# Optimization experiments

Measured on AMD Instinct MI355X. Metric: run time of the kernel, lower is better.

## Reference

```python
import jax, jax.numpy as jnp
import numpy as np

THETA = 0.5
STRIDE = 2
HEADS = 4
D_K = 32
D_V = 32
EPS = 1e-5


def pdc_conv(x, w, stride, theta=THETA):
    """Conv_PDC: (Co,Ci,1,8) weight -> 3x3 kernel with zero center, minus theta * 1x1 sum conv."""
    Co, Ci = w.shape[0], w.shape[1]
    w8 = w[:, :, 0, :]  # (Co, Ci, 8)
    w9 = jnp.concatenate(
        [w8[:, :, :4], jnp.zeros((Co, Ci, 1), w.dtype), w8[:, :, 4:]], axis=2
    ).reshape(Co, Ci, 3, 3)
    dn = jax.lax.conv_dimension_numbers(x.shape, w9.shape, ('NCHW', 'OIHW', 'NCHW'))
    out_n = jax.lax.conv_general_dilated(x, w9, (stride, stride), [(1, 1), (1, 1)], dimension_numbers=dn)
    kd = jnp.sum(w8, axis=2)[:, :, None, None]  # (Co, Ci, 1, 1)
    out_d = jax.lax.conv_general_dilated(x, kd, (stride, stride), [(0, 0), (0, 0)], dimension_numbers=dn)
    return out_n - theta * out_d


def full_layer_norm(x):
    # F.layer_norm(x, x.shape): normalize over ALL dims (incl. batch), no affine
    m = jnp.mean(x)
    v = jnp.mean(jnp.square(x - m))
    return (x - m) * jax.lax.rsqrt(v + EPS)


def setup_inputs() -> dict:
    key = jax.random.key(0)
    ks = jax.random.split(key, 12)
    b, c, h, w = 8, 64, 64, 64
    hd = HEADS * D_K  # 128
    s = 0.05
    return {
        'x': jax.random.normal(ks[0], (b, c, h, w), jnp.float32),
        'wk': jax.random.normal(ks[1], (c, c, 1, 8), jnp.float32) * s,
        'wv': jax.random.normal(ks[2], (c, c, 1, 8), jnp.float32) * s,
        'fcq_w': jax.random.normal(ks[3], (hd, c), jnp.float32) * s,
        'fcq_b': jax.random.normal(ks[4], (hd,), jnp.float32) * s,
        'fck_w': jax.random.normal(ks[5], (hd, c), jnp.float32) * s,
        'fck_b': jax.random.normal(ks[6], (hd,), jnp.float32) * s,
        'fcv_w': jax.random.normal(ks[7], (hd, c), jnp.float32) * s,
        'fcv_b': jax.random.normal(ks[8], (hd,), jnp.float32) * s,
        'fco_w': jax.random.normal(ks[9], (c, hd), jnp.float32) * s,
        'fco_b': jax.random.normal(ks[10], (c,), jnp.float32) * s,
        'B': jax.random.normal(ks[11], (1, HEADS, h * w, (h // STRIDE) * (w // STRIDE)), jnp.float32) * s,
    }


def reference(x, wk, wv, fcq_w, fcq_b, fck_w, fck_b, fcv_w, fcv_b, fco_w, fco_b, B):
    b, c, h, w = x.shape
    hw = h * w
    xr = jnp.transpose(x.reshape(b, c, hw), (0, 2, 1))  # (b, hw, c)
    xr = full_layer_norm(xr)

    q = xr @ fcq_w.T + fcq_b                    # (b, hw, H*dk)
    q = jnp.transpose(q.reshape(b, hw, HEADS, D_K), (0, 2, 1, 3))  # (b,H,hw,dk)

    k = pdc_conv(x, wk, STRIDE)                 # (b, c, h2, w2)
    kb, kc, kh, kw = k.shape
    k = jnp.transpose(k.reshape(kb, kc, kh * kw), (0, 2, 1)) @ fck_w.T + fck_b
    k = jnp.transpose(k.reshape(kb, kh * kw, HEADS, D_K), (0, 2, 1, 3))  # (b,H,n2,dk)

    v = pdc_conv(x, wv, STRIDE)
    vb, vc, vh, vw = v.shape
    v = jnp.transpose(v.reshape(vb, vc, vh * vw), (0, 2, 1)) @ fcv_w.T + fcv_b
    v = jnp.transpose(v.reshape(vb, vh * vw, HEADS, D_V), (0, 2, 1, 3))  # (b,H,n2,dv)

    attn = jnp.einsum('bhid,bhjd->bhij', q, k) * (D_K ** -0.5) + B
    attn = jax.nn.softmax(attn, axis=-1)
    out = jnp.einsum('bhij,bhjd->bhid', attn, v)            # (b,H,hw,dv)
    out = jnp.transpose(out, (0, 2, 1, 3)).reshape(b, hw, HEADS * D_V)
    out = out @ fco_w.T + fco_b                              # (b, hw, c)
    # Faithful to source: .view(b, channels, h, w) without permute
    out = out.reshape(b, c, h, w)
    return out + x
```

## Files before the change

### kernel.cpp

```cpp
#include <hip/hip_runtime.h>
#include <cmath>

#define THETA 0.5f
#define EPS 1e-5f

typedef __attribute__((ext_vector_type(8))) short bf16x8;
typedef __attribute__((ext_vector_type(4))) float f32x4;
typedef __attribute__((ext_vector_type(4))) unsigned u32x4;

__device__ inline unsigned short f2b(float f) {
  unsigned u = __builtin_bit_cast(unsigned, f);
  return (unsigned short)((u + 0x7fffu + ((u >> 16) & 1u)) >> 16);
}
__device__ inline float b2f(unsigned short u) {
  unsigned v = (unsigned)u << 16;
  return __builtin_bit_cast(float, v);
}
__device__ inline float blo(unsigned u) { return __builtin_bit_cast(float, u << 16); }
__device__ inline float bhi(unsigned u) { return __builtin_bit_cast(float, u & 0xffff0000u); }
__device__ inline float exp2fast(float x) {
  float r;
  asm("v_exp_f32 %0, %1" : "=v"(r) : "v"(x));
  return r;
}
__device__ inline unsigned cvtpk(float lo, float hi) {
  unsigned r;
  asm("v_cvt_pk_bf16_f32 %0, %1, %2" : "=v"(r) : "v"(lo), "v"(hi));
  return r;
}

__global__ __launch_bounds__(256) void pre_kernel(
    const float* __restrict__ B, unsigned short* __restrict__ B2, int nB4,
    const float* __restrict__ x, float* __restrict__ stats, int nx4) {
  int bx = blockIdx.x;
  if (bx < 2048) {
    int tid = bx * 256 + threadIdx.x;
    int stride = 2048 * 256;
    const float4* b4 = (const float4*)B;
    const float L = 1.4426950408889634f;
    for (int i = tid; i < nB4; i += stride) {
      float4 v = b4[i];
      unsigned lo = f2b(v.x * L) | ((unsigned)f2b(v.y * L) << 16);
      unsigned hi = f2b(v.z * L) | ((unsigned)f2b(v.w * L) << 16);
      *(uint2*)(B2 + (size_t)i * 4) = make_uint2(lo, hi);
    }
  } else {
    int sb = bx - 2048;
    int tid = sb * 256 + threadIdx.x;
    int stride = 512 * 256;
    float s = 0.f, ss = 0.f;
    const float4* x4 = (const float4*)x;
    for (int i = tid; i < nx4; i += stride) {
      float4 v = x4[i];
      s  += v.x + v.y + v.z + v.w;
      ss += v.x * v.x + v.y * v.y + v.z * v.z + v.w * v.w;
    }
    for (int off = 32; off; off >>= 1) {
      s  += __shfl_down(s, off);
      ss += __shfl_down(ss, off);
    }
    __shared__ float ls[4], lss[4];
    int lane = threadIdx.x & 63, wid = threadIdx.x >> 6;
    if (lane == 0) { ls[wid] = s; lss[wid] = ss; }
    __syncthreads();
    if (threadIdx.x == 0) {
      float a = 0.f, b = 0.f;
      for (int w = 0; w < 4; ++w) { a += ls[w]; b += lss[w]; }
      stats[2 * sb]     = a;
      stats[2 * sb + 1] = b;
    }
  }
}

__global__ __launch_bounds__(256) void pdc_conv_kernel(
    const float* __restrict__ x,
    const float* __restrict__ wk,
    const float* __restrict__ wv,
    float* __restrict__ Kc,
    float* __restrict__ Vc) {
  int oh  = blockIdx.x;
  int coh = blockIdx.y;
  int bb  = blockIdx.z;
  __shared__ float xs[64][3][64];
  const float* xb = x + (size_t)bb * 262144;
  int r1 = 2 * oh;
  for (int i = 0; i < 48; ++i) {
    int idx = threadIdx.x + i * 256;
    int ci = idx / 192;
    int rem = idx - ci * 192;
    int r = rem >> 6, col = rem & 63;
    int row = r1 - 1 + r;
    xs[ci][r][col] = (row >= 0) ? xb[((size_t)ci * 64 + row) * 64 + col] : 0.f;
  }
  __syncthreads();
  int owl = threadIdx.x & 7;
  int co  = coh * 32 + (threadIdx.x >> 3);
  int c0 = owl * 8;
  int ecol = c0 ? c0 - 1 : 0;
  float accK[4] = {0.f, 0.f, 0.f, 0.f}, accV[4] = {0.f, 0.f, 0.f, 0.f};
  const float* wkc = wk + (size_t)co * 512;
  const float* wvc = wv + (size_t)co * 512;
  for (int ci = 0; ci < 64; ++ci) {
    float4 k0 = *(const float4*)(wkc + ci * 8);
    float4 k1 = *(const float4*)(wkc + ci * 8 + 4);
    float4 v0 = *(const float4*)(wvc + ci * 8);
    float4 v1 = *(const float4*)(wvc + ci * 8 + 4);
    float kdk = k0.x + k0.y + k0.z + k0.w + k1.x + k1.y + k1.z + k1.w;
    float kdv = v0.x + v0.y + v0.z + v0.w + v1.x + v1.y + v1.z + v1.w;
    float wK[9] = {k0.x, k0.y, k0.z, k0.w, -THETA * kdk, k1.x, k1.y, k1.z, k1.w};
    float wV[9] = {v0.x, v0.y, v0.z, v0.w, -THETA * kdv, v1.x, v1.y, v1.z, v1.w};
    float xr[3][9];
#pragma unroll
    for (int r = 0; r < 3; ++r) {
      float ev = owl ? xs[ci][r][ecol] : 0.f;
      float4 a = *(const float4*)&xs[ci][r][c0];
      float4 b = *(const float4*)&xs[ci][r][c0 + 4];
      xr[r][0] = ev;
      xr[r][1] = a.x; xr[r][2] = a.y; xr[r][3] = a.z; xr[r][4] = a.w;
      xr[r][5] = b.x; xr[r][6] = b.y; xr[r][7] = b.z; xr[r][8] = b.w;
    }
#pragma unroll
    for (int ky = 0; ky < 3; ++ky)
#pragma unroll
      for (int kx = 0; kx < 3; ++kx) {
        float wkk = wK[ky * 3 + kx], wvv = wV[ky * 3 + kx];
#pragma unroll
        for (int i = 0; i < 4; ++i) {
          float xv = xr[ky][2 * i + kx];
          accK[i] = fmaf(wkk, xv, accK[i]);
          accV[i] = fmaf(wvv, xv, accV[i]);
        }
      }
  }
  size_t o = ((size_t)bb * 64 + co) * 1024 + oh * 32 + owl * 4;
  *(float4*)&Kc[o] = make_float4(accK[0], accK[1], accK[2], accK[3]);
  *(float4*)&Vc[o] = make_float4(accV[0], accV[1], accV[2], accV[3]);
}

__global__ __launch_bounds__(256) void proj_mfma_kernel(
    const float* __restrict__ x, const float* __restrict__ Kc, const float* __restrict__ Vc,
    const float* __restrict__ Wq, const float* __restrict__ bq,
    const float* __restrict__ Wk, const float* __restrict__ bk,
    const float* __restrict__ Wv, const float* __restrict__ bv,
    unsigned short* __restrict__ Qb, unsigned short* __restrict__ Kb,
    unsigned short* __restrict__ Vtb, const float* __restrict__ stats) {
  int bx = blockIdx.x;
  const float* A; const float* W; const float* bias; unsigned short* outp;
  int R, doLN, transp, r0, bb;
  if (bx < 512) {
    A = x; W = Wq; bias = bq; outp = Qb; R = 4096; doLN = 1; transp = 0;
    bb = bx >> 6; r0 = (bx & 63) * 64;
  } else {
    int i = bx - 512; int kv = i >> 7; int j = i & 127;
    bb = j >> 4; r0 = (j & 15) * 64; R = 1024; doLN = 0;
    if (!kv) { A = Kc; W = Wk; bias = bk; outp = Kb;  transp = 0; }
    else     { A = Vc; W = Wv; bias = bv; outp = Vtb; transp = 1; }
  }
  int tid = threadIdx.x;
  int w = tid >> 6, lane = tid & 63, g = lane >> 4, li = lane & 15;

  float m = 0.f, rs = 1.f;
  if (doLN) {
    const float2* sp = (const float2*)stats;
    float2 a = sp[tid];
    float2 b2 = sp[tid + 256];
    float s = a.x + b2.x, ss = a.y + b2.y;
    for (int off = 32; off; off >>= 1) {
      s  += __shfl_down(s, off);
      ss += __shfl_down(ss, off);
    }
    __shared__ float red[8];
    int lane0 = tid & 63, wid0 = tid >> 6;
    if (lane0 == 0) { red[wid0] = s; red[4 + wid0] = ss; }
    __syncthreads();
    float ts  = red[0] + red[1] + red[2] + red[3];
    float tss = red[4] + red[5] + red[6] + red[7];
    const float inv = 1.0f / 2097152.0f;
    m = ts * inv;
    float v = tss * inv - m * m;
    rs = rsqrtf(v + EPS);
    __syncthreads();
  }

  bf16x8 wf[2][2];
#pragma unroll
  for (int dd = 0; dd < 2; ++dd)
#pragma unroll
    for (int kh = 0; kh < 2; ++kh) {
      const float* wp = W + (size_t)(w * 32 + dd * 16 + li) * 64 + kh * 32 + g * 8;
      float4 w0 = *(const float4*)wp;
      float4 w1 = *(const float4*)(wp + 4);
      u32x4 u;
      u[0] = cvtpk(w0.x, w0.y); u[1] = cvtpk(w0.z, w0.w);
      u[2] = cvtpk(w1.x, w1.y); u[3] = cvtpk(w1.z, w1.w);
      wf[dd][kh] = __builtin_bit_cast(bf16x8, u);
    }

  __shared__ __align__(16) unsigned short As2[64][72];
  const float* Ab = A + (size_t)bb * 64 * R;
  for (int i = 0; i < 16; ++i) {
    int idx = tid + i * 256;
    int c = idx >> 6, r = idx & 63;
    float v = Ab[(size_t)c * R + r0 + r];
    if (doLN) v = (v - m) * rs;
    As2[r][c] = f2b(v);
  }
  __syncthreads();

  f32x4 acc[2][4];
#pragma unroll
  for (int dd = 0; dd < 2; ++dd)
#pragma unroll
    for (int rt = 0; rt < 4; ++rt) acc[dd][rt] = (f32x4){0.f, 0.f, 0.f, 0.f};

#pragma unroll
  for (int rt = 0; rt < 4; ++rt) {
    bf16x8 xf0 = *(const bf16x8*)&As2[rt * 16 + li][g * 8];
    bf16x8 xf1 = *(const bf16x8*)&As2[rt * 16 + li][32 + g * 8];
    if (!transp) {
#pragma unroll
      for (int dd = 0; dd < 2; ++dd) {
        acc[dd][rt] = __builtin_amdgcn_mfma_f32_16x16x32_bf16(wf[dd][0], xf0, acc[dd][rt], 0, 0, 0);
        acc[dd][rt] = __builtin_amdgcn_mfma_f32_16x16x32_bf16(wf[dd][1], xf1, acc[dd][rt], 0, 0, 0);
      }
    } else {
#pragma unroll
      for (int dd = 0; dd < 2; ++dd) {
        acc[dd][rt] = __builtin_amdgcn_mfma_f32_16x16x32_bf16(xf0, wf[dd][0], acc[dd][rt], 0, 0, 0);
        acc[dd][rt] = __builtin_amdgcn_mfma_f32_16x16x32_bf16(xf1, wf[dd][1], acc[dd][rt], 0, 0, 0);
      }
    }
  }

  size_t bh = (size_t)bb * 4 + w;
  if (!transp) {
#pragma unroll
    for (int dd = 0; dd < 2; ++dd) {
      float4 b4 = *(const float4*)(bias + w * 32 + dd * 16 + g * 4);
#pragma unroll
      for (int rt = 0; rt < 4; ++rt) {
        f32x4 a = acc[dd][rt];
        unsigned lo = cvtpk(a[0] + b4.x, a[1] + b4.y);
        unsigned hi = cvtpk(a[2] + b4.z, a[3] + b4.w);
        int r = r0 + rt * 16 + li;
        *(uint2*)(outp + (bh * R + r) * 32 + dd * 16 + g * 4) = make_uint2(lo, hi);
      }
    }
  } else {
#pragma unroll
    for (int dd = 0; dd < 2; ++dd) {
      float bsc = bias[w * 32 + dd * 16 + li];
#pragma unroll
      for (int rt = 0; rt < 4; ++rt) {
        f32x4 a = acc[dd][rt];
        unsigned lo = cvtpk(a[0] + bsc, a[1] + bsc);
        unsigned hi = cvtpk(a[2] + bsc, a[3] + bsc);
        *(uint2*)(outp + (bh * 32 + dd * 16 + li) * (size_t)R + r0 + rt * 16 + g * 4) =
            make_uint2(lo, hi);
      }
    }
  }
}

__global__ __launch_bounds__(256, 4) void attn_mfma_kernel(
    const unsigned short* __restrict__ Qb,
    const unsigned short* __restrict__ Kb,
    const unsigned short* __restrict__ Vtb,
    const unsigned short* __restrict__ B2,
    unsigned short* __restrict__ Ob) {
  int qt = blockIdx.x;
  int b  = blockIdx.y & 7;
  int h  = blockIdx.y >> 3;
  int tid = threadIdx.x;
  int w = tid >> 6, lane = tid & 63, g = lane >> 4, li = lane & 15;

  __shared__ __align__(16) unsigned short Ks[4096];
  __shared__ __align__(16) unsigned short Vs[4096];

  size_t bh = (size_t)b * 4 + h;
  int q0 = qt * 128 + w * 32;
  bf16x8 qfA = *(const bf16x8*)(Qb + (bh * 4096 + q0 + li) * 32 + g * 8);
  bf16x8 qfB = *(const bf16x8*)(Qb + (bh * 4096 + q0 + 16 + li) * 32 + g * 8);
  const unsigned short* BpA = B2 + ((size_t)h * 4096 + q0 + li) * 1024;
  const unsigned short* BpB = BpA + 16 * 1024;
  const unsigned short* Kg = Kb + bh * 32768;
  const unsigned short* Vg = Vtb + bh * 32768;

  float rsumA = 0.f, rsumB = 0.f;
  f32x4 accA0 = {0.f, 0.f, 0.f, 0.f}, accA1 = {0.f, 0.f, 0.f, 0.f};
  f32x4 accB0 = {0.f, 0.f, 0.f, 0.f}, accB1 = {0.f, 0.f, 0.f, 0.f};
  const float scale2 = 0.17677669529663687f * 1.4426950408889634f;

  int krow = tid >> 1, khalf = tid & 1;
  int j5 = krow & 31;
  int jp = (krow & ~31) | (((j5 >> 2) & 1) << 4) | (((j5 >> 3) & 3) << 2) | (j5 & 3);
  const int kc0 = ((jp >> 4) * 64 + khalf * 32 + (jp & 15)) * 8;
  int vr = tid >> 3, sg = tid & 7;
  const int vc0 = (((sg >> 1) * 2 + (vr >> 4)) * 64 + (sg & 1) * 32 + (vr & 15)) * 8;

  for (int jc = 0; jc < 1024; jc += 128) {
    __syncthreads();
    {
      const uint4* ks = (const uint4*)(Kg + (size_t)(jc + krow) * 32 + khalf * 16);
      *(uint4*)&Ks[kc0]       = ks[0];
      *(uint4*)&Ks[kc0 + 128] = ks[1];
      const uint4* vs = (const uint4*)(Vg + (size_t)vr * 1024 + jc + sg * 16);
      *(uint4*)&Vs[vc0]       = vs[0];
      *(uint4*)&Vs[vc0 + 128] = vs[1];
    }
    __syncthreads();

#pragma unroll
    for (int js = 0; js < 4; ++js) {
      bf16x8 kf0 = *(const bf16x8*)&Ks[((js * 2) * 64 + lane) * 8];
      bf16x8 kf1 = *(const bf16x8*)&Ks[((js * 2 + 1) * 64 + lane) * 8];
      const f32x4 z = {0.f, 0.f, 0.f, 0.f};
      f32x4 sA0 = __builtin_amdgcn_mfma_f32_16x16x32_bf16(kf0, qfA, z, 0, 0, 0);
      f32x4 sB0 = __builtin_amdgcn_mfma_f32_16x16x32_bf16(kf0, qfB, z, 0, 0, 0);
      f32x4 sA1 = __builtin_amdgcn_mfma_f32_16x16x32_bf16(kf1, qfA, z, 0, 0, 0);
      f32x4 sB1 = __builtin_amdgcn_mfma_f32_16x16x32_bf16(kf1, qfB, z, 0, 0, 0);

      u32x4 bA = *(const u32x4*)(BpA + jc + js * 32 + g * 8);
      u32x4 bB = *(const u32x4*)(BpB + jc + js * 32 + g * 8);

      float pA[8], pB[8];
      pA[0] = exp2fast(fmaf(sA0[0], scale2, blo(bA[0])));
      pA[1] = exp2fast(fmaf(sA0[1], scale2, bhi(bA[0])));
      pA[2] = exp2fast(fmaf(sA0[2], scale2, blo(bA[1])));
      pA[3] = exp2fast(fmaf(sA0[3], scale2, bhi(bA[1])));
      pA[4] = exp2fast(fmaf(sA1[0], scale2, blo(bA[2])));
      pA[5] = exp2fast(fmaf(sA1[1], scale2, bhi(bA[2])));
      pA[6] = exp2fast(fmaf(sA1[2], scale2, blo(bA[3])));
      pA[7] = exp2fast(fmaf(sA1[3], scale2, bhi(bA[3])));
      pB[0] = exp2fast(fmaf(sB0[0], scale2, blo(bB[0])));
      pB[1] = exp2fast(fmaf(sB0[1], scale2, bhi(bB[0])));
      pB[2] = exp2fast(fmaf(sB0[2], scale2, blo(bB[1])));
      pB[3] = exp2fast(fmaf(sB0[3], scale2, bhi(bB[1])));
      pB[4] = exp2fast(fmaf(sB1[0], scale2, blo(bB[2])));
      pB[5] = exp2fast(fmaf(sB1[1], scale2, bhi(bB[2])));
      pB[6] = exp2fast(fmaf(sB1[2], scale2, blo(bB[3])));
      pB[7] = exp2fast(fmaf(sB1[3], scale2, bhi(bB[3])));

      rsumA += ((pA[0] + pA[1]) + (pA[2] + pA[3])) + ((pA[4] + pA[5]) + (pA[6] + pA[7]));
      rsumB += ((pB[0] + pB[1]) + (pB[2] + pB[3])) + ((pB[4] + pB[5]) + (pB[6] + pB[7]));

      u32x4 wA, wB;
      wA[0] = cvtpk(pA[0], pA[1]); wA[1] = cvtpk(pA[2], pA[3]);
      wA[2] = cvtpk(pA[4], pA[5]); wA[3] = cvtpk(pA[6], pA[7]);
      wB[0] = cvtpk(pB[0], pB[1]); wB[1] = cvtpk(pB[2], pB[3]);
      wB[2] = cvtpk(pB[4], pB[5]); wB[3] = cvtpk(pB[6], pB[7]);
      bf16x8 paA = __builtin_bit_cast(bf16x8, wA);
      bf16x8 paB = __builtin_bit_cast(bf16x8, wB);

      bf16x8 vf0 = *(const bf16x8*)&Vs[(js * 128 + lane) * 8];
      bf16x8 vf1 = *(const bf16x8*)&Vs[((js * 2 + 1) * 64 + lane) * 8];
      accA0 = __builtin_amdgcn_mfma_f32_16x16x32_bf16(paA, vf0, accA0, 0, 0, 0);
      accA1 = __builtin_amdgcn_mfma_f32_16x16x32_bf16(paA, vf1, accA1, 0, 0, 0);
      accB0 = __builtin_amdgcn_mfma_f32_16x16x32_bf16(paB, vf0, accB0, 0, 0, 0);
      accB1 = __builtin_amdgcn_mfma_f32_16x16x32_bf16(paB, vf1, accB1, 0, 0, 0);
    }
  }

  rsumA += __shfl_xor(rsumA, 16);
  rsumA += __shfl_xor(rsumA, 32);
  rsumB += __shfl_xor(rsumB, 16);
  rsumB += __shfl_xor(rsumB, 32);
  float invA = 1.0f / rsumA;
  float invB = 1.0f / rsumB;
  float invqA[4], invqB[4];
#pragma unroll
  for (int r = 0; r < 4; ++r) {
    invqA[r] = __shfl(invA, g * 4 + r);
    invqB[r] = __shfl(invB, g * 4 + r);
  }

#pragma unroll
  for (int r = 0; r < 4; ++r) {
    size_t rowA = (size_t)b * 4096 + q0 + g * 4 + r;
    Ob[rowA * 128 + h * 32 + li]      = f2b(accA0[r] * invqA[r]);
    Ob[rowA * 128 + h * 32 + 16 + li] = f2b(accA1[r] * invqA[r]);
    size_t rowB = rowA + 16;
    Ob[rowB * 128 + h * 32 + li]      = f2b(accB0[r] * invqB[r]);
    Ob[rowB * 128 + h * 32 + 16 + li] = f2b(accB1[r] * invqB[r]);
  }
}

__global__ __launch_bounds__(256) void outproj_mfma_kernel(
    const unsigned short* __restrict__ O,
    const float* __restrict__ Wo,
    const float* __restrict__ bo,
    const float* __restrict__ x,
    float* __restrict__ out) {
  int pb = blockIdx.x & 127;
  int bb = blockIdx.x >> 7;
  int tid = threadIdx.x;
  int w = tid >> 6, lane = tid & 63, g = lane >> 4, li = lane & 15;
  int p0 = pb * 32;

  bf16x8 wf[4];
#pragma unroll
  for (int kt = 0; kt < 4; ++kt) {
    const float* wp = Wo + (size_t)(w * 16 + li) * 128 + kt * 32 + g * 8;
    float4 w0 = *(const float4*)wp;
    float4 w1 = *(const float4*)(wp + 4);
    u32x4 u;
    u[0] = cvtpk(w0.x, w0.y); u[1] = cvtpk(w0.z, w0.w);
    u[2] = cvtpk(w1.x, w1.y); u[3] = cvtpk(w1.z, w1.w);
    wf[kt] = __builtin_bit_cast(bf16x8, u);
  }

  f32x4 acc[2];
#pragma unroll
  for (int pt = 0; pt < 2; ++pt) acc[pt] = (f32x4){0.f, 0.f, 0.f, 0.f};

#pragma unroll
  for (int pt = 0; pt < 2; ++pt) {
    const unsigned short* Op = O + ((size_t)bb * 4096 + p0 + pt * 16 + li) * 128;
    bf16x8 of0 = *(const bf16x8*)(Op + g * 8);
    bf16x8 of1 = *(const bf16x8*)(Op + 32 + g * 8);
    bf16x8 of2 = *(const bf16x8*)(Op + 64 + g * 8);
    bf16x8 of3 = *(const bf16x8*)(Op + 96 + g * 8);
    acc[pt] = __builtin_amdgcn_mfma_f32_16x16x32_bf16(wf[0], of0, acc[pt], 0, 0, 0);
    acc[pt] = __builtin_amdgcn_mfma_f32_16x16x32_bf16(wf[1], of1, acc[pt], 0, 0, 0);
    acc[pt] = __builtin_amdgcn_mfma_f32_16x16x32_bf16(wf[2], of2, acc[pt], 0, 0, 0);
    acc[pt] = __builtin_amdgcn_mfma_f32_16x16x32_bf16(wf[3], of3, acc[pt], 0, 0, 0);
  }

  float4 bo4 = *(const float4*)(bo + w * 16 + g * 4);
#pragma unroll
  for (int pt = 0; pt < 2; ++pt) {
    int p = p0 + pt * 16 + li;
    size_t base = (size_t)bb * 262144 + (size_t)p * 64 + w * 16 + g * 4;
    float4 xr = *(const float4*)(x + base);
    float4 o;
    o.x = acc[pt][0] + bo4.x + xr.x;
    o.y = acc[pt][1] + bo4.y + xr.y;
    o.z = acc[pt][2] + bo4.z + xr.z;
    o.w = acc[pt][3] + bo4.w + xr.w;
    *(float4*)(out + base) = o;
  }
}

extern "C" void kernel_launch(void* const* d_in, const int* in_sizes, int n_in,
                              void* d_out, int out_size, void* d_ws, size_t ws_size,
                              hipStream_t stream) {
  const float* x    = (const float*)d_in[0];
  const float* wk   = (const float*)d_in[1];
  const float* wv   = (const float*)d_in[2];
  const float* fcqw = (const float*)d_in[3];
  const float* fcqb = (const float*)d_in[4];
  const float* fckw = (const float*)d_in[5];
  const float* fckb = (const float*)d_in[6];
  const float* fcvw = (const float*)d_in[7];
  const float* fcvb = (const float*)d_in[8];
  const float* fcow = (const float*)d_in[9];
  const float* fcob = (const float*)d_in[10];
  const float* Bb   = (const float*)d_in[11];
  float* out = (float*)d_out;
  float* ws  = (float*)d_ws;

  float* stats = ws;
  float* Kc = ws + 1024;
  float* Vc = Kc + 524288;
  unsigned short* B2  = (unsigned short*)(Vc + 524288);
  unsigned short* Qb  = B2 + 16777216;
  unsigned short* Kb  = Qb + 4194304;
  unsigned short* Vtb = Kb + 1048576;
  unsigned short* Ob  = Vtb + 1048576;

  pre_kernel<<<dim3(2560), dim3(256), 0, stream>>>(Bb, B2, 4194304, x, stats, 524288);
  pdc_conv_kernel<<<dim3(32, 2, 8), dim3(256), 0, stream>>>(x, wk, wv, Kc, Vc);
  proj_mfma_kernel<<<dim3(768), dim3(256), 0, stream>>>(
      x, Kc, Vc, fcqw, fcqb, fckw, fckb, fcvw, fcvb, Qb, Kb, Vtb, stats);
  attn_mfma_kernel<<<dim3(32, 32), dim3(256), 0, stream>>>(Qb, Kb, Vtb, B2, Ob);
  outproj_mfma_kernel<<<dim3(1024), dim3(256), 0, stream>>>(Ob, fcow, fcob, x, out);
}
```

Before: 229.0 us.

## Fuse PDC conv with K/V projection using bf16 MFMA implicit GEMM

Replaces the scalar fp32 PDC convolution kernel with an MFMA implicit-GEMM conv that reads bf16-transposed input tiles from LDS. The conv is fused with the K/V linear projections, so the fp32 Kc/Vc intermediates no longer round-trip through global memory. Conv weights are pre-packed to bf16 in extra blocks of the pre kernel, and the Q projection becomes its own specialised kernel. The cost is bf16 rounding of the conv inputs and weights, plus an intermediate bf16 rounding of the conv output before projection, which may reduce accuracy.

```diff
diff --git a/kernel.cpp b/kernel.cpp
--- a/kernel.cpp
+++ b/kernel.cpp
@@ -31,7 +31,9 @@
 
 __global__ __launch_bounds__(256) void pre_kernel(
     const float* __restrict__ B, unsigned short* __restrict__ B2, int nB4,
-    const float* __restrict__ x, float* __restrict__ stats, int nx4) {
+    const float* __restrict__ x, float* __restrict__ stats, int nx4,
+    const float* __restrict__ wk, const float* __restrict__ wv,
+    unsigned short* __restrict__ w9t) {
   int bx = blockIdx.x;
   if (bx < 2048) {
     int tid = bx * 256 + threadIdx.x;
@@ -44,7 +46,7 @@
       unsigned hi = f2b(v.z * L) | ((unsigned)f2b(v.w * L) << 16);
       *(uint2*)(B2 + (size_t)i * 4) = make_uint2(lo, hi);
     }
-  } else {
+  } else if (bx < 2560) {
     int sb = bx - 2048;
     int tid = sb * 256 + threadIdx.x;
     int stride = 512 * 256;
@@ -69,125 +71,159 @@
       stats[2 * sb]     = a;
       stats[2 * sb + 1] = b;
     }
-  }
-}
-
-__global__ __launch_bounds__(256) void pdc_conv_kernel(
+  } else {
+    int t = (bx - 2560) * 256 + threadIdx.x;
+    int kern = t >> 12, co = (t >> 6) & 63, ci = t & 63;
+    const float* w8 = (kern ? wv : wk) + ((size_t)co * 64 + ci) * 8;
+    float4 a = *(const float4*)w8;
+    float4 b = *(const float4*)(w8 + 4);
+    float s = (a.x + a.y + a.z + a.w) + (b.x + b.y + b.z + b.w);
+    unsigned short* o = w9t + (size_t)(kern * 64 + co) * 576 + ci;
+    o[0]       = f2b(a.x);
+    o[64]      = f2b(a.y);
+    o[128]     = f2b(a.z);
+    o[192]     = f2b(a.w);
+    o[256]     = f2b(-THETA * s);
+    o[320]     = f2b(b.x);
+    o[384]     = f2b(b.y);
+    o[448]     = f2b(b.z);
+    o[512]     = f2b(b.w);
+  }
+}
+
+__global__ __launch_bounds__(256) void convproj_kernel(
     const float* __restrict__ x,
-    const float* __restrict__ wk,
-    const float* __restrict__ wv,
-    float* __restrict__ Kc,
-    float* __restrict__ Vc) {
-  int oh  = blockIdx.x;
-  int coh = blockIdx.y;
-  int bb  = blockIdx.z;
-  __shared__ float xs[64][3][64];
-  const float* xb = x + (size_t)bb * 262144;
-  int r1 = 2 * oh;
-  for (int i = 0; i < 48; ++i) {
-    int idx = threadIdx.x + i * 256;
-    int ci = idx / 192;
-    int rem = idx - ci * 192;
-    int r = rem >> 6, col = rem & 63;
-    int row = r1 - 1 + r;
-    xs[ci][r][col] = (row >= 0) ? xb[((size_t)ci * 64 + row) * 64 + col] : 0.f;
-  }
-  __syncthreads();
-  int owl = threadIdx.x & 7;
-  int co  = coh * 32 + (threadIdx.x >> 3);
-  int c0 = owl * 8;
-  int ecol = c0 ? c0 - 1 : 0;
-  float accK[4] = {0.f, 0.f, 0.f, 0.f}, accV[4] = {0.f, 0.f, 0.f, 0.f};
-  const float* wkc = wk + (size_t)co * 512;
-  const float* wvc = wv + (size_t)co * 512;
-  for (int ci = 0; ci < 64; ++ci) {
-    float4 k0 = *(const float4*)(wkc + ci * 8);
-    float4 k1 = *(const float4*)(wkc + ci * 8 + 4);
-    float4 v0 = *(const float4*)(wvc + ci * 8);
-    float4 v1 = *(const float4*)(wvc + ci * 8 + 4);
-    float kdk = k0.x + k0.y + k0.z + k0.w + k1.x + k1.y + k1.z + k1.w;
-    float kdv = v0.x + v0.y + v0.z + v0.w + v1.x + v1.y + v1.z + v1.w;
-    float wK[9] = {k0.x, k0.y, k0.z, k0.w, -THETA * kdk, k1.x, k1.y, k1.z, k1.w};
-    float wV[9] = {v0.x, v0.y, v0.z, v0.w, -THETA * kdv, v1.x, v1.y, v1.z, v1.w};
-    float xr[3][9];
-#pragma unroll
-    for (int r = 0; r < 3; ++r) {
-      float ev = owl ? xs[ci][r][ecol] : 0.f;
-      float4 a = *(const float4*)&xs[ci][r][c0];
-      float4 b = *(const float4*)&xs[ci][r][c0 + 4];
-      xr[r][0] = ev;
-      xr[r][1] = a.x; xr[r][2] = a.y; xr[r][3] = a.z; xr[r][4] = a.w;
-      xr[r][5] = b.x; xr[r][6] = b.y; xr[r][7] = b.z; xr[r][8] = b.w;
-    }
-#pragma unroll
-    for (int ky = 0; ky < 3; ++ky)
-#pragma unroll
-      for (int kx = 0; kx < 3; ++kx) {
-        float wkk = wK[ky * 3 + kx], wvv = wV[ky * 3 + kx];
-#pragma unroll
-        for (int i = 0; i < 4; ++i) {
-          float xv = xr[ky][2 * i + kx];
-          accK[i] = fmaf(wkk, xv, accK[i]);
-          accV[i] = fmaf(wvv, xv, accV[i]);
-        }
-      }
-  }
-  size_t o = ((size_t)bb * 64 + co) * 1024 + oh * 32 + owl * 4;
-  *(float4*)&Kc[o] = make_float4(accK[0], accK[1], accK[2], accK[3]);
-  *(float4*)&Vc[o] = make_float4(accV[0], accV[1], accV[2], accV[3]);
-}
-
-__global__ __launch_bounds__(256) void proj_mfma_kernel(
-    const float* __restrict__ x, const float* __restrict__ Kc, const float* __restrict__ Vc,
-    const float* __restrict__ Wq, const float* __restrict__ bq,
+    const unsigned short* __restrict__ w9t,
     const float* __restrict__ Wk, const float* __restrict__ bk,
     const float* __restrict__ Wv, const float* __restrict__ bv,
-    unsigned short* __restrict__ Qb, unsigned short* __restrict__ Kb,
-    unsigned short* __restrict__ Vtb, const float* __restrict__ stats) {
-  int bx = blockIdx.x;
-  const float* A; const float* W; const float* bias; unsigned short* outp;
-  int R, doLN, transp, r0, bb;
-  if (bx < 512) {
-    A = x; W = Wq; bias = bq; outp = Qb; R = 4096; doLN = 1; transp = 0;
-    bb = bx >> 6; r0 = (bx & 63) * 64;
-  } else {
-    int i = bx - 512; int kv = i >> 7; int j = i & 127;
-    bb = j >> 4; r0 = (j & 15) * 64; R = 1024; doLN = 0;
-    if (!kv) { A = Kc; W = Wk; bias = bk; outp = Kb;  transp = 0; }
-    else     { A = Vc; W = Wv; bias = bv; outp = Vtb; transp = 1; }
-  }
+    unsigned short* __restrict__ Kb,
+    unsigned short* __restrict__ Vtb) {
+  int owh = blockIdx.x & 1;
+  int oh  = (blockIdx.x >> 1) & 31;
+  int bb  = blockIdx.x >> 6;
   int tid = threadIdx.x;
   int w = tid >> 6, lane = tid & 63, g = lane >> 4, li = lane & 15;
 
-  float m = 0.f, rs = 1.f;
-  if (doLN) {
-    const float2* sp = (const float2*)stats;
-    float2 a = sp[tid];
-    float2 b2 = sp[tid + 256];
-    float s = a.x + b2.x, ss = a.y + b2.y;
-    for (int off = 32; off; off >>= 1) {
-      s  += __shfl_down(s, off);
-      ss += __shfl_down(ss, off);
-    }
-    __shared__ float red[8];
-    int lane0 = tid & 63, wid0 = tid >> 6;
-    if (lane0 == 0) { red[wid0] = s; red[4 + wid0] = ss; }
-    __syncthreads();
-    float ts  = red[0] + red[1] + red[2] + red[3];
-    float tss = red[4] + red[5] + red[6] + red[7];
-    const float inv = 1.0f / 2097152.0f;
-    m = ts * inv;
-    float v = tss * inv - m * m;
-    rs = rsqrtf(v + EPS);
-    __syncthreads();
-  }
+  __shared__ __align__(16) unsigned short xsT[3][36][72];
+  __shared__ __align__(16) unsigned short ctK[16][72];
+  __shared__ __align__(16) unsigned short ctV[16][72];
+
+  const float* xb = x + (size_t)bb * 262144;
+  int g0 = owh * 32 - 4;
+  int rbase = 2 * oh - 1;
+  for (int i = 0; i < 27; ++i) {
+    int idx = tid + i * 256;
+    int ci = idx / 108;
+    int rem = idx - ci * 108;
+    int rr = rem / 36, cc = rem - rr * 36;
+    int row = rbase + rr, col = g0 + cc;
+    float v = (row >= 0 && col >= 0) ? xb[((size_t)ci * 64 + row) * 64 + col] : 0.f;
+    xsT[rr][cc][ci] = f2b(v);
+  }
+  __syncthreads();
+
+  f32x4 aK = {0.f, 0.f, 0.f, 0.f}, aV = {0.f, 0.f, 0.f, 0.f};
+#pragma unroll
+  for (int t = 0; t < 9; ++t) {
+    int ky = t / 3, kx = t - ky * 3;
+    int cc = 2 * li + 3 + kx;
+#pragma unroll
+    for (int kh = 0; kh < 2; ++kh) {
+      bf16x8 bfrag = *(const bf16x8*)&xsT[ky][cc][kh * 32 + g * 8];
+      bf16x8 ak = *(const bf16x8*)(w9t + (size_t)(w * 16 + li) * 576 + t * 64 + kh * 32 + g * 8);
+      bf16x8 av = *(const bf16x8*)(w9t + (size_t)(64 + w * 16 + li) * 576 + t * 64 + kh * 32 + g * 8);
+      aK = __builtin_amdgcn_mfma_f32_16x16x32_bf16(ak, bfrag, aK, 0, 0, 0);
+      aV = __builtin_amdgcn_mfma_f32_16x16x32_bf16(av, bfrag, aV, 0, 0, 0);
+    }
+  }
+  *(uint2*)&ctK[li][w * 16 + g * 4] = make_uint2(cvtpk(aK[0], aK[1]), cvtpk(aK[2], aK[3]));
+  *(uint2*)&ctV[li][w * 16 + g * 4] = make_uint2(cvtpk(aV[0], aV[1]), cvtpk(aV[2], aV[3]));
+  __syncthreads();
+
+  bf16x8 wfK[2][2], wfV[2][2];
+#pragma unroll
+  for (int dd = 0; dd < 2; ++dd)
+#pragma unroll
+    for (int kh = 0; kh < 2; ++kh) {
+      const float* wp = Wk + (size_t)(w * 32 + dd * 16 + li) * 64 + kh * 32 + g * 8;
+      float4 w0 = *(const float4*)wp;
+      float4 w1 = *(const float4*)(wp + 4);
+      u32x4 u;
+      u[0] = cvtpk(w0.x, w0.y); u[1] = cvtpk(w0.z, w0.w);
+      u[2] = cvtpk(w1.x, w1.y); u[3] = cvtpk(w1.z, w1.w);
+      wfK[dd][kh] = __builtin_bit_cast(bf16x8, u);
+      const float* vp = Wv + (size_t)(w * 32 + dd * 16 + li) * 64 + kh * 32 + g * 8;
+      float4 v0 = *(const float4*)vp;
+      float4 v1 = *(const float4*)(vp + 4);
+      u[0] = cvtpk(v0.x, v0.y); u[1] = cvtpk(v0.z, v0.w);
+      u[2] = cvtpk(v1.x, v1.y); u[3] = cvtpk(v1.z, v1.w);
+      wfV[dd][kh] = __builtin_bit_cast(bf16x8, u);
+    }
+
+  f32x4 pK[2] = {{0.f, 0.f, 0.f, 0.f}, {0.f, 0.f, 0.f, 0.f}};
+  f32x4 pV[2] = {{0.f, 0.f, 0.f, 0.f}, {0.f, 0.f, 0.f, 0.f}};
+#pragma unroll
+  for (int kh = 0; kh < 2; ++kh) {
+    bf16x8 bK  = *(const bf16x8*)&ctK[li][kh * 32 + g * 8];
+    bf16x8 aVc = *(const bf16x8*)&ctV[li][kh * 32 + g * 8];
+#pragma unroll
+    for (int dd = 0; dd < 2; ++dd) {
+      pK[dd] = __builtin_amdgcn_mfma_f32_16x16x32_bf16(wfK[dd][kh], bK, pK[dd], 0, 0, 0);
+      pV[dd] = __builtin_amdgcn_mfma_f32_16x16x32_bf16(aVc, wfV[dd][kh], pV[dd], 0, 0, 0);
+    }
+  }
+
+  size_t bh = (size_t)bb * 4 + w;
+  int pos0 = oh * 32 + owh * 16;
+#pragma unroll
+  for (int dd = 0; dd < 2; ++dd) {
+    float4 b4 = *(const float4*)(bk + w * 32 + dd * 16 + g * 4);
+    uint2 st = make_uint2(cvtpk(pK[dd][0] + b4.x, pK[dd][1] + b4.y),
+                          cvtpk(pK[dd][2] + b4.z, pK[dd][3] + b4.w));
+    *(uint2*)(Kb + (bh * 1024 + pos0 + li) * 32 + dd * 16 + g * 4) = st;
+    float bsc = bv[w * 32 + dd * 16 + li];
+    uint2 sv = make_uint2(cvtpk(pV[dd][0] + bsc, pV[dd][1] + bsc),
+                          cvtpk(pV[dd][2] + bsc, pV[dd][3] + bsc));
+    *(uint2*)(Vtb + (bh * 32 + dd * 16 + li) * 1024 + pos0 + g * 4) = sv;
+  }
+}
+
+__global__ __launch_bounds__(256) void projq_kernel(
+    const float* __restrict__ x, const float* __restrict__ Wq,
+    const float* __restrict__ bq, unsigned short* __restrict__ Qb,
+    const float* __restrict__ stats) {
+  int bx = blockIdx.x;
+  int bb = bx >> 6, r0 = (bx & 63) * 64;
+  const int R = 4096;
+  int tid = threadIdx.x;
+  int w = tid >> 6, lane = tid & 63, g = lane >> 4, li = lane & 15;
+
+  const float2* sp = (const float2*)stats;
+  float2 a = sp[tid];
+  float2 b2 = sp[tid + 256];
+  float s = a.x + b2.x, ss = a.y + b2.y;
+  for (int off = 32; off; off >>= 1) {
+    s  += __shfl_down(s, off);
+    ss += __shfl_down(ss, off);
+  }
+  __shared__ float red[8];
+  int lane0 = tid & 63, wid0 = tid >> 6;
+  if (lane0 == 0) { red[wid0] = s; red[4 + wid0] = ss; }
+  __syncthreads();
+  float ts  = red[0] + red[1] + red[2] + red[3];
+  float tss = red[4] + red[5] + red[6] + red[7];
+  const float inv = 1.0f / 2097152.0f;
+  float m = ts * inv;
+  float v0 = tss * inv - m * m;
+  float rs = rsqrtf(v0 + EPS);
+  __syncthreads();
 
   bf16x8 wf[2][2];
 #pragma unroll
   for (int dd = 0; dd < 2; ++dd)
 #pragma unroll
     for (int kh = 0; kh < 2; ++kh) {
-      const float* wp = W + (size_t)(w * 32 + dd * 16 + li) * 64 + kh * 32 + g * 8;
+      const float* wp = Wq + (size_t)(w * 32 + dd * 16 + li) * 64 + kh * 32 + g * 8;
       float4 w0 = *(const float4*)wp;
       float4 w1 = *(const float4*)(wp + 4);
       u32x4 u;
@@ -197,13 +233,12 @@
     }
 
   __shared__ __align__(16) unsigned short As2[64][72];
-  const float* Ab = A + (size_t)bb * 64 * R;
+  const float* Ab = x + (size_t)bb * 64 * R;
   for (int i = 0; i < 16; ++i) {
     int idx = tid + i * 256;
     int c = idx >> 6, r = idx & 63;
     float v = Ab[(size_t)c * R + r0 + r];
-    if (doLN) v = (v - m) * rs;
-    As2[r][c] = f2b(v);
+    As2[r][c] = f2b((v - m) * rs);
   }
   __syncthreads();
 
@@ -217,47 +252,24 @@
   for (int rt = 0; rt < 4; ++rt) {
     bf16x8 xf0 = *(const bf16x8*)&As2[rt * 16 + li][g * 8];
     bf16x8 xf1 = *(const bf16x8*)&As2[rt * 16 + li][32 + g * 8];
-    if (!transp) {
-#pragma unroll
-      for (int dd = 0; dd < 2; ++dd) {
-        acc[dd][rt] = __builtin_amdgcn_mfma_f32_16x16x32_bf16(wf[dd][0], xf0, acc[dd][rt], 0, 0, 0);
-        acc[dd][rt] = __builtin_amdgcn_mfma_f32_16x16x32_bf16(wf[dd][1], xf1, acc[dd][rt], 0, 0, 0);
-      }
-    } else {
-#pragma unroll
-      for (int dd = 0; dd < 2; ++dd) {
-        acc[dd][rt] = __builtin_amdgcn_mfma_f32_16x16x32_bf16(xf0, wf[dd][0], acc[dd][rt], 0, 0, 0);
-        acc[dd][rt] = __builtin_amdgcn_mfma_f32_16x16x32_bf16(xf1, wf[dd][1], acc[dd][rt], 0, 0, 0);
-      }
+#pragma unroll
+    for (int dd = 0; dd < 2; ++dd) {
+      acc[dd][rt] = __builtin_amdgcn_mfma_f32_16x16x32_bf16(wf[dd][0], xf0, acc[dd][rt], 0, 0, 0);
+      acc[dd][rt] = __builtin_amdgcn_mfma_f32_16x16x32_bf16(wf[dd][1], xf1, acc[dd][rt], 0, 0, 0);
     }
   }
 
   size_t bh = (size_t)bb * 4 + w;
-  if (!transp) {
-#pragma unroll
-    for (int dd = 0; dd < 2; ++dd) {
-      float4 b4 = *(const float4*)(bias + w * 32 + dd * 16 + g * 4);
-#pragma unroll
-      for (int rt = 0; rt < 4; ++rt) {
-        f32x4 a = acc[dd][rt];
-        unsigned lo = cvtpk(a[0] + b4.x, a[1] + b4.y);
-        unsigned hi = cvtpk(a[2] + b4.z, a[3] + b4.w);
-        int r = r0 + rt * 16 + li;
-        *(uint2*)(outp + (bh * R + r) * 32 + dd * 16 + g * 4) = make_uint2(lo, hi);
-      }
-    }
-  } else {
-#pragma unroll
-    for (int dd = 0; dd < 2; ++dd) {
-      float bsc = bias[w * 32 + dd * 16 + li];
-#pragma unroll
-      for (int rt = 0; rt < 4; ++rt) {
-        f32x4 a = acc[dd][rt];
-        unsigned lo = cvtpk(a[0] + bsc, a[1] + bsc);
-        unsigned hi = cvtpk(a[2] + bsc, a[3] + bsc);
-        *(uint2*)(outp + (bh * 32 + dd * 16 + li) * (size_t)R + r0 + rt * 16 + g * 4) =
-            make_uint2(lo, hi);
-      }
+#pragma unroll
+  for (int dd = 0; dd < 2; ++dd) {
+    float4 b4 = *(const float4*)(bq + w * 32 + dd * 16 + g * 4);
+#pragma unroll
+    for (int rt = 0; rt < 4; ++rt) {
+      f32x4 a2 = acc[dd][rt];
+      unsigned lo = cvtpk(a2[0] + b4.x, a2[1] + b4.y);
+      unsigned hi = cvtpk(a2[2] + b4.z, a2[3] + b4.w);
+      int r = r0 + rt * 16 + li;
+      *(uint2*)(Qb + (bh * (size_t)R + r) * 32 + dd * 16 + g * 4) = make_uint2(lo, hi);
     }
   }
 }
@@ -460,18 +472,18 @@
   float* ws  = (float*)d_ws;
 
   float* stats = ws;
-  float* Kc = ws + 1024;
-  float* Vc = Kc + 524288;
-  unsigned short* B2  = (unsigned short*)(Vc + 524288);
+  unsigned short* w9t = (unsigned short*)(ws + 1024);
+  unsigned short* B2  = w9t + 73728;
   unsigned short* Qb  = B2 + 16777216;
   unsigned short* Kb  = Qb + 4194304;
   unsigned short* Vtb = Kb + 1048576;
   unsigned short* Ob  = Vtb + 1048576;
 
-  pre_kernel<<<dim3(2560), dim3(256), 0, stream>>>(Bb, B2, 4194304, x, stats, 524288);
-  pdc_conv_kernel<<<dim3(32, 2, 8), dim3(256), 0, stream>>>(x, wk, wv, Kc, Vc);
-  proj_mfma_kernel<<<dim3(768), dim3(256), 0, stream>>>(
-      x, Kc, Vc, fcqw, fcqb, fckw, fckb, fcvw, fcvb, Qb, Kb, Vtb, stats);
+  pre_kernel<<<dim3(2592), dim3(256), 0, stream>>>(Bb, B2, 4194304, x, stats, 524288,
+                                                   wk, wv, w9t);
+  convproj_kernel<<<dim3(512), dim3(256), 0, stream>>>(x, w9t, fckw, fckb, fcvw, fcvb,
+                                                       Kb, Vtb);
+  projq_kernel<<<dim3(512), dim3(256), 0, stream>>>(x, fcqw, fcqb, Qb, stats);
   attn_mfma_kernel<<<dim3(32, 32), dim3(256), 0, stream>>>(Qb, Kb, Vtb, B2, Ob);
   outproj_mfma_kernel<<<dim3(1024), dim3(256), 0, stream>>>(Ob, fcow, fcob, x, out);
 }
```

New measurement: 207.5 us. 9.4% less time.
